# Kernel optimization log

Measured on AMD Instinct MI355X. Metric: run time of the kernel, lower is better.

Reference implementation:

```python
import jax, jax.numpy as jnp
import numpy as np

B, S, HID = 2, 2048, 2048
N_HEADS, N_KV = 16, 4
HEAD_DIM = HID // N_HEADS  # 128
N_REP = N_HEADS // N_KV
ROPE_THETA = 1000000.0


def setup_inputs() -> dict:
    key = jax.random.key(0)
    ks = jax.random.split(key, 8)
    s = 0.02
    # causal additive mask: 0 on/below diagonal, large negative above
    neg = jnp.finfo(jnp.float32).min
    causal = jnp.where(jnp.tril(jnp.ones((S, S), dtype=bool)), 0.0, neg)
    attention_mask = jnp.broadcast_to(causal[None, None], (B, 1, S, S)).astype(jnp.float32)
    return {
        "hidden_states": jax.random.normal(ks[0], (B, S, HID), jnp.float32),
        "Wq": jax.random.normal(ks[1], (HID, HID), jnp.float32) * s,
        "bq": jax.random.normal(ks[2], (HID,), jnp.float32) * s,
        "Wk": jax.random.normal(ks[3], (N_KV * HEAD_DIM, HID), jnp.float32) * s,
        "bk": jax.random.normal(ks[4], (N_KV * HEAD_DIM,), jnp.float32) * s,
        "Wv": jax.random.normal(ks[5], (N_KV * HEAD_DIM, HID), jnp.float32) * s,
        "bv": jax.random.normal(ks[6], (N_KV * HEAD_DIM,), jnp.float32) * s,
        "attention_mask": attention_mask,
        "position_ids": jnp.broadcast_to(jnp.arange(S, dtype=jnp.int64)[None], (B, S)),
    }


def _rotate_half(x):
    x1, x2 = jnp.split(x, 2, axis=-1)
    return jnp.concatenate((-x2, x1), axis=-1)


def _rope_cos_sin(position_ids, dtype):
    inv_freq = 1.0 / (ROPE_THETA ** (jnp.arange(0, HEAD_DIM, 2, dtype=jnp.float32) / HEAD_DIM))
    freqs = position_ids.astype(jnp.float32)[:, :, None] * inv_freq[None, None, :]  # [B,S,hd/2]
    emb = jnp.concatenate((freqs, freqs), axis=-1)  # [B,S,hd]
    return jnp.cos(emb).astype(dtype), jnp.sin(emb).astype(dtype)


def reference(hidden_states, Wq, bq, Wk, bk, Wv, bv, attention_mask, position_ids):
    b, s, _ = hidden_states.shape
    q = (hidden_states @ Wq.T + bq).reshape(b, s, N_HEADS, HEAD_DIM).transpose(0, 2, 1, 3)
    k = (hidden_states @ Wk.T + bk).reshape(b, s, N_KV, HEAD_DIM).transpose(0, 2, 1, 3)
    v = (hidden_states @ Wv.T + bv).reshape(b, s, N_KV, HEAD_DIM).transpose(0, 2, 1, 3)

    cos, sin = _rope_cos_sin(position_ids, hidden_states.dtype)
    cos, sin = cos[:, None], sin[:, None]  # unsqueeze head dim
    q = q * cos + _rotate_half(q) * sin
    k = k * cos + _rotate_half(k) * sin

    # GQA: repeat kv heads
    k = jnp.repeat(k, N_REP, axis=1)
    v = jnp.repeat(v, N_REP, axis=1)

    scores = jnp.einsum('bhqd,bhkd->bhqk', q, k) / jnp.sqrt(jnp.float32(HEAD_DIM)).astype(q.dtype)
    scores = scores + attention_mask
    probs = jax.nn.softmax(scores.astype(jnp.float32), axis=-1).astype(q.dtype)
    out = jnp.einsum('bhqk,bhkd->bhqd', probs, v)  # [B,H,S,hd]
    return out.transpose(0, 2, 1, 3).reshape(b, s, HID)
```

## Files before the change

### kernel.cpp

```cpp
#include <hip/hip_runtime.h>
#include <hip/hip_bf16.h>

typedef short bf16x8 __attribute__((ext_vector_type(8)));
typedef float f32x4 __attribute__((ext_vector_type(4)));
typedef unsigned int u32;
typedef unsigned short u16;

#define SLEN 2048
#define LOG2S 11

__device__ __forceinline__ u16 f2bf(float x) {
  u32 u = __builtin_bit_cast(u32, x);
  u = (u + 0x7fffu + ((u >> 16) & 1u)) >> 16;
  return (u16)u;
}

__device__ __forceinline__ u32 pkbf(float a, float b) {
  return (u32)f2bf(a) | ((u32)f2bf(b) << 16);
}

__device__ __forceinline__ void gload16(const void* g, void* l) {
  __builtin_amdgcn_global_load_lds((const __attribute__((address_space(1))) u32*)g,
                                   (__attribute__((address_space(3))) u32*)l, 16, 0, 0);
}

#define MFMA16(a, b, c) __builtin_amdgcn_mfma_f32_16x16x32_bf16((a), (b), (c), 0, 0, 0)

__global__ void k_convert4(const float* __restrict__ s0, u16* __restrict__ d0,
                           const float* __restrict__ s1, u16* __restrict__ d1,
                           const float* __restrict__ s2, u16* __restrict__ d2,
                           const float* __restrict__ s3, u16* __restrict__ d3) {
  const int n0 = 2097152, n1 = 1048576, n2 = 262144, n3 = 262144;
  const int total = n0 + n1 + n2 + n3;
  int i = blockIdx.x * blockDim.x + threadIdx.x;
  int stride = gridDim.x * blockDim.x;
  for (; i < total; i += stride) {
    const float* s; u16* d; int j = i;
    if (j < n0) { s = s0; d = d0; }
    else if ((j -= n0) < n1) { s = s1; d = d1; }
    else if ((j -= n1) < n2) { s = s2; d = d2; }
    else { j -= n2; s = s3; d = d3; }
    float4 v = reinterpret_cast<const float4*>(s)[j];
    ushort4 o;
    o.x = f2bf(v.x); o.y = f2bf(v.y); o.z = f2bf(v.z); o.w = f2bf(v.w);
    reinterpret_cast<ushort4*>(d)[j] = o;
  }
}

__global__ void k_rope_table(float* __restrict__ ctab, float* __restrict__ stab) {
  int i = blockIdx.x * blockDim.x + threadIdx.x;
  int s = i >> 6, d = i & 63;
  float invf = powf(1.0e6f, -(float)d * (1.0f / 64.0f));
  float a = (float)s * invf;
  ctab[i] = cosf(a);
  stab[i] = sinf(a);
}

__global__ __launch_bounds__(256, 2) void k_proj(
    const u16* __restrict__ Xb, const u16* __restrict__ Wqb,
    const u16* __restrict__ Wkb, const u16* __restrict__ Wvb,
    const float* __restrict__ bq, const float* __restrict__ bk, const float* __restrict__ bv,
    const float* __restrict__ ctab, const float* __restrict__ stab,
    u16* __restrict__ Qb, u16* __restrict__ Kb, u16* __restrict__ Vt) {
  __shared__ __align__(16) char smb[65536];
  const int tid = threadIdx.x;
  const int lane = tid & 63;
  const int w = tid >> 6;
  const int l15 = lane & 15, g = lane >> 4;
  const int m0 = blockIdx.x * 128;
  const int y = blockIdx.y;
  int mode, head;
  const u16* W; const float* bias;
  if (y < 16)      { mode = 0; head = y;      W = Wqb; bias = bq; }
  else if (y < 20) { mode = 1; head = y - 16; W = Wkb; bias = bk; }
  else             { mode = 2; head = y - 20; W = Wvb; bias = bv; }
  const int n0 = head * 128;

  f32x4 acc[2][8] = {};

  const char* asrc[4]; const char* bsrc[4]; int ldo[4];
  #pragma unroll
  for (int it = 0; it < 4; ++it) {
    int c = it * 256 + tid;
    int row = c >> 3;
    int inner = ((c & 7) << 4) ^ ((row & 7) << 4);
    asrc[it] = (const char*)Xb + ((size_t)(m0 + row) * 2048) * 2 + inner;
    bsrc[it] = (const char*)W  + ((size_t)(n0 + row) * 2048) * 2 + inner;
    ldo[it] = c * 16;
  }

  auto STAGE = [&](int buf, int t) {
    char* ad = smb + buf * 16384;
    char* bd = smb + 32768 + buf * 16384;
    #pragma unroll
    for (int it = 0; it < 4; ++it) gload16(asrc[it] + t * 128, ad + ldo[it]);
    #pragma unroll
    for (int it = 0; it < 4; ++it) gload16(bsrc[it] + t * 128, bd + ldo[it]);
  };

  STAGE(0, 0);
  int cur = 0;
  for (int t = 0; t < 32; ++t) {
    if (t + 1 < 32) {
      STAGE(cur ^ 1, t + 1);
      asm volatile("s_waitcnt vmcnt(8)" ::: "memory");
    } else {
      asm volatile("s_waitcnt vmcnt(0)" ::: "memory");
    }
    __builtin_amdgcn_s_barrier();
    asm volatile("" ::: "memory");
    const char* Ac = smb + cur * 16384;
    const char* Bc = smb + 32768 + cur * 16384;
    #pragma unroll
    for (int kf = 0; kf < 2; ++kf) {
      const int innerk = kf * 64 + g * 16;
      const int rowA0 = w * 32 + l15;
      const int rowA1 = rowA0 + 16;
      bf16x8 a0 = *(const bf16x8*)(Ac + rowA0 * 128 + (innerk ^ ((rowA0 & 7) << 4)));
      bf16x8 a1 = *(const bf16x8*)(Ac + rowA1 * 128 + (innerk ^ ((rowA1 & 7) << 4)));
      #pragma unroll
      for (int j = 0; j < 8; ++j) {
        const int rowB = j * 16 + l15;
        bf16x8 bb = *(const bf16x8*)(Bc + rowB * 128 + (innerk ^ ((rowB & 7) << 4)));
        acc[0][j] = MFMA16(a0, bb, acc[0][j]);
        acc[1][j] = MFMA16(a1, bb, acc[1][j]);
      }
    }
    asm volatile("" ::: "memory");
    __builtin_amdgcn_s_barrier();
    cur ^= 1;
  }

  float biasv[8];
  #pragma unroll
  for (int j = 0; j < 8; ++j) biasv[j] = bias[n0 + j * 16 + l15];

  #pragma unroll
  for (int i = 0; i < 2; ++i) {
    #pragma unroll
    for (int r = 0; r < 4; ++r) {
      const int m = m0 + w * 32 + i * 16 + g * 4 + r;
      const int b = m >> LOG2S, s = m & (SLEN - 1);
      float v[8];
      #pragma unroll
      for (int j = 0; j < 8; ++j) v[j] = acc[i][j][r] + biasv[j];
      if (mode <= 1) {
        #pragma unroll
        for (int j = 0; j < 4; ++j) {
          const int f = j * 16 + l15;
          const float cv = ctab[s * 64 + f];
          const float sv = stab[s * 64 + f];
          const float lo = v[j], hi = v[j + 4];
          v[j]     = lo * cv - hi * sv;
          v[j + 4] = hi * cv + lo * sv;
        }
      }
      if (mode == 0) {
        #pragma unroll
        for (int j = 0; j < 8; ++j) v[j] *= 0.08838834764831845f;
        u16* dst = Qb + (((size_t)(b * 16 + head) * SLEN + s) * 128);
        #pragma unroll
        for (int j = 0; j < 8; ++j) dst[j * 16 + l15] = f2bf(v[j]);
      } else if (mode == 1) {
        u16* dst = Kb + (((size_t)(b * 4 + head) * SLEN + s) * 128);
        #pragma unroll
        for (int j = 0; j < 8; ++j) dst[j * 16 + l15] = f2bf(v[j]);
      } else {
        const int sl = w * 32 + i * 16 + g * 4 + r;
        #pragma unroll
        for (int j = 0; j < 8; ++j) {
          const int d = j * 16 + l15;
          *(u16*)(smb + d * 256 + ((sl * 2) ^ ((d & 7) << 4))) = f2bf(v[j]);
        }
      }
    }
  }
  if (mode == 2) {
    __syncthreads();
    const int sbase = m0 & (SLEN - 1);
    const int bidx = m0 >> LOG2S;
    u16* Vg = Vt + ((size_t)(bidx * 4 + head) * 128) * SLEN;
    #pragma unroll
    for (int itr = 0; itr < 8; ++itr) {
      int c = itr * 256 + tid;
      int d = c >> 4, sc = c & 15;
      bf16x8 val = *(const bf16x8*)(smb + d * 256 + ((sc * 16) ^ ((d & 7) << 4)));
      *(bf16x8*)(Vg + (size_t)d * SLEN + sbase + sc * 8) = val;
    }
  }
}

__global__ __launch_bounds__(256, 3) void k_attn(
    const u16* __restrict__ Qb, const u16* __restrict__ Kb, const u16* __restrict__ Vt,
    float* __restrict__ Out) {
  __shared__ __align__(16) char smb[49152];
  const int tid = threadIdx.x, lane = tid & 63, w = tid >> 6;
  const int l15 = lane & 15, g = lane >> 4;
  const int lid = blockIdx.y * 16 + blockIdx.x;
  const int sl = lid >> 3;
  const int bh = (lid & 7) * 4 + (sl & 3);
  const int qb_t = sl >> 2;
  const int qa_t = 31 - qb_t;
  const int b = bh >> 4, h = bh & 15, kv = h >> 2;
  const u16* Qbase = Qb + ((size_t)(b * 16 + h) * SLEN) * 128;
  const char* Kg = (const char*)(Kb + ((size_t)(b * 4 + kv) * SLEN) * 128);
  const char* Vg = (const char*)(Vt + ((size_t)(b * 4 + kv) * 128) * SLEN);
  char* Pwa = smb + 32768 + w * 4096;
  char* Pwb = Pwa + 2048;

  const char* srcK[2]; const char* srcV[2]; int ldoK[2], ldoV[2];
  #pragma unroll
  for (int it = 0; it < 2; ++it) {
    int c = it * 256 + tid;
    ldoK[it] = c * 16; ldoV[it] = c * 16;
    int rk = c >> 4;
    srcK[it] = Kg + (size_t)rk * 256 + (((c & 15) << 4) ^ ((rk & 7) << 4));
    int rv = c >> 2;
    srcV[it] = Vg + (size_t)rv * (SLEN * 2) + (((c & 3) << 4) ^ (((rv >> 1) & 3) << 4));
  }

  const int qwa = qa_t * 64 + w * 16, qwb = qb_t * 64 + w * 16;
  bf16x8 qfa[4], qfb[4];
  #pragma unroll
  for (int kf = 0; kf < 4; ++kf) {
    qfa[kf] = *(const bf16x8*)(Qbase + (size_t)(qwa + l15) * 128 + kf * 32 + g * 8);
    qfb[kf] = *(const bf16x8*)(Qbase + (size_t)(qwb + l15) * 128 + kf * 32 + g * 8);
  }

  float ma = -1e30f, la = 0.f, mb = -1e30f, lb = 0.f;
  f32x4 oa[8] = {}, ob[8] = {};
  const int nt = 2 * qa_t + 2;

  auto STAGE = [&](int buf, int t) {
    char* kd = smb + buf * 8192;
    char* vd = smb + 16384 + buf * 8192;
    const size_t koK = (size_t)t * 8192;
    const size_t koV = (size_t)t * 64;
    #pragma unroll
    for (int it = 0; it < 2; ++it) gload16(srcK[it] + koK, kd + ldoK[it]);
    #pragma unroll
    for (int it = 0; it < 2; ++it) gload16(srcV[it] + koV, vd + ldoV[it]);
  };

  auto softmax = [&](f32x4* sc, float& m, float& l, f32x4* oacc, char* Pdst,
                     int k0, int qw, bool maskneed) {
    float sv[8];
    #pragma unroll
    for (int n = 0; n < 2; ++n) {
      #pragma unroll
      for (int r = 0; r < 4; ++r) {
        float x = sc[n][r];
        if (maskneed && (k0 + n * 16 + g * 4 + r > qw + l15)) x = -1e30f;
        sv[n * 4 + r] = x;
      }
    }
    float tm = fmaxf(fmaxf(fmaxf(sv[0], sv[1]), fmaxf(sv[2], sv[3])),
                     fmaxf(fmaxf(sv[4], sv[5]), fmaxf(sv[6], sv[7])));
    tm = fmaxf(tm, __shfl_xor(tm, 16));
    tm = fmaxf(tm, __shfl_xor(tm, 32));
    if (__any(tm > m + 8.0f)) {
      float mnew = fmaxf(m, tm);
      float alpha = __expf(m - mnew);
      m = mnew;
      l *= alpha;
      #pragma unroll
      for (int r = 0; r < 4; ++r) {
        float ar = __shfl(alpha, g * 4 + r);
        #pragma unroll
        for (int nf = 0; nf < 8; ++nf) oacc[nf][r] *= ar;
      }
    }
    float p[8];
    #pragma unroll
    for (int i2 = 0; i2 < 8; ++i2) p[i2] = __expf(sv[i2] - m);
    float ts = ((p[0] + p[1]) + (p[2] + p[3])) + ((p[4] + p[5]) + (p[6] + p[7]));
    ts += __shfl_xor(ts, 16);
    ts += __shfl_xor(ts, 32);
    l += ts;
    #pragma unroll
    for (int n = 0; n < 2; ++n) {
      uint2 pk;
      pk.x = pkbf(p[n * 4 + 0], p[n * 4 + 1]);
      pk.y = pkbf(p[n * 4 + 2], p[n * 4 + 3]);
      *(uint2*)(Pdst + l15 * 128 + ((n * 32 + g * 8) ^ ((l15 & 7) << 4))) = pk;
    }
  };

  STAGE(0, 0);
  int cur = 0;
  for (int t = 0; t < nt; ++t) {
    if (t + 1 < nt) {
      STAGE(cur ^ 1, t + 1);
      asm volatile("s_waitcnt vmcnt(4)" ::: "memory");
    } else {
      asm volatile("s_waitcnt vmcnt(0)" ::: "memory");
    }
    __builtin_amdgcn_s_barrier();
    asm volatile("" ::: "memory");
    const char* Kc = smb + cur * 8192;
    const char* Vc = smb + 16384 + cur * 8192;
    const int k0 = t * 32;
    const bool act_a = (k0 <= qwa + 15);
    const bool act_b = (t < 2 * qb_t + 2) && (k0 <= qwb + 15);

    if (act_a | act_b) {
      f32x4 sa[2] = {}, sb[2] = {};
      #pragma unroll
      for (int kf = 0; kf < 4; ++kf) {
        #pragma unroll
        for (int n = 0; n < 2; ++n) {
          const int row = n * 16 + l15;
          bf16x8 kb = *(const bf16x8*)(Kc + row * 256 + ((kf * 64 + g * 16) ^ ((row & 7) << 4)));
          if (act_a) sa[n] = MFMA16(kb, qfa[kf], sa[n]);
          if (act_b) sb[n] = MFMA16(kb, qfb[kf], sb[n]);
        }
      }
      if (act_a) softmax(sa, ma, la, oa, Pwa, k0, qwa, k0 + 31 > qwa);
      if (act_b) softmax(sb, mb, lb, ob, Pwb, k0, qwb, k0 + 31 > qwb);

      bf16x8 paa = {}, pab = {};
      if (act_a) paa = *(const bf16x8*)(Pwa + l15 * 128 + ((g * 16) ^ ((l15 & 7) << 4)));
      if (act_b) pab = *(const bf16x8*)(Pwb + l15 * 128 + ((g * 16) ^ ((l15 & 7) << 4)));
      #pragma unroll
      for (int nf = 0; nf < 8; ++nf) {
        const int row = nf * 16 + l15;
        bf16x8 vb = *(const bf16x8*)(Vc + row * 64 + ((g * 16) ^ (((row >> 1) & 3) << 4)));
        if (act_a) oa[nf] = MFMA16(paa, vb, oa[nf]);
        if (act_b) ob[nf] = MFMA16(pab, vb, ob[nf]);
      }
    }
    asm volatile("" ::: "memory");
    __builtin_amdgcn_s_barrier();
    cur ^= 1;
  }

  float lia = 1.0f / la, lib = 1.0f / lb;
  #pragma unroll
  for (int r = 0; r < 4; ++r) {
    float inv = __shfl(lia, g * 4 + r);
    const int q = qwa + g * 4 + r;
    float* dst = Out + ((size_t)(b * SLEN + q) * 2048) + h * 128;
    #pragma unroll
    for (int nf = 0; nf < 8; ++nf) dst[nf * 16 + l15] = oa[nf][r] * inv;
  }
  #pragma unroll
  for (int r = 0; r < 4; ++r) {
    float inv = __shfl(lib, g * 4 + r);
    const int q = qwb + g * 4 + r;
    float* dst = Out + ((size_t)(b * SLEN + q) * 2048) + h * 128;
    #pragma unroll
    for (int nf = 0; nf < 8; ++nf) dst[nf * 16 + l15] = ob[nf][r] * inv;
  }
}

extern "C" void kernel_launch(void* const* d_in, const int* in_sizes, int n_in,
                              void* d_out, int out_size, void* d_ws, size_t ws_size,
                              hipStream_t stream) {
  const float* X  = (const float*)d_in[0];
  const float* Wq = (const float*)d_in[1];
  const float* bq = (const float*)d_in[2];
  const float* Wk = (const float*)d_in[3];
  const float* bk = (const float*)d_in[4];
  const float* Wv = (const float*)d_in[5];
  const float* bv = (const float*)d_in[6];
  float* Out = (float*)d_out;
  char* ws = (char*)d_ws;
  u16* Xb    = (u16*)(ws + 0);
  u16* Wqb   = (u16*)(ws + 16777216);
  u16* Wkb   = (u16*)(ws + 25165824);
  u16* Wvb   = (u16*)(ws + 27262976);
  u16* Qb    = (u16*)(ws + 29360128);
  u16* Kb    = (u16*)(ws + 46137344);
  u16* Vt    = (u16*)(ws + 50331648);
  float* ctab = (float*)(ws + 54525952);
  float* stab = (float*)(ws + 55050240);

  hipLaunchKernelGGL(k_convert4, dim3(2048), dim3(256), 0, stream,
                     X, Xb, Wq, Wqb, Wk, Wkb, Wv, Wvb);
  hipLaunchKernelGGL(k_rope_table, dim3(512), dim3(256), 0, stream, ctab, stab);
  hipLaunchKernelGGL(k_proj, dim3(32, 24), dim3(256), 0, stream,
                     Xb, Wqb, Wkb, Wvb, bq, bk, bv, ctab, stab, Qb, Kb, Vt);
  hipLaunchKernelGGL(k_attn, dim3(16, 32), dim3(256), 0, stream, Qb, Kb, Vt, Out);
}
```

Before: 291.3 us.

## Split paired causal q-tiles into one tile per block, longest first

The attention kernel used to pair a long and a short causal query tile in each block so every block did balanced work. It now gives each block a single 64-row query tile across 1024 blocks. Blocks are ordered longest tile first, and the grid is arranged so the four query heads sharing a KV head launch next to each other for L2 reuse. The P scratch and register state are halved, so LDS drops to 36 KB and launch bounds rise to 4 blocks per CU. The cost is that each block now streams K/V without sharing it across two query tiles, which doubles K/V loads per unit of work.

```diff
diff --git a/kernel.cpp b/kernel.cpp
--- a/kernel.cpp
+++ b/kernel.cpp
@@ -190,46 +190,43 @@
   }
 }
 
-__global__ __launch_bounds__(256, 3) void k_attn(
+__global__ __launch_bounds__(256, 4) void k_attn(
     const u16* __restrict__ Qb, const u16* __restrict__ Kb, const u16* __restrict__ Vt,
     float* __restrict__ Out) {
-  __shared__ __align__(16) char smb[49152];
+  __shared__ __align__(16) char smb[36864];
   const int tid = threadIdx.x, lane = tid & 63, w = tid >> 6;
   const int l15 = lane & 15, g = lane >> 4;
-  const int lid = blockIdx.y * 16 + blockIdx.x;
-  const int sl = lid >> 3;
-  const int bh = (lid & 7) * 4 + (sl & 3);
-  const int qb_t = sl >> 2;
-  const int qa_t = 31 - qb_t;
-  const int b = bh >> 4, h = bh & 15, kv = h >> 2;
+  const int x = blockIdx.x;
+  const int y = blockIdx.y;
+  const int b = x >> 2, kv = x & 3;
+  const int hr = y & 3;
+  const int qt = 31 - (y >> 2);
+  const int h = kv * 4 + hr;
   const u16* Qbase = Qb + ((size_t)(b * 16 + h) * SLEN) * 128;
   const char* Kg = (const char*)(Kb + ((size_t)(b * 4 + kv) * SLEN) * 128);
   const char* Vg = (const char*)(Vt + ((size_t)(b * 4 + kv) * 128) * SLEN);
-  char* Pwa = smb + 32768 + w * 4096;
-  char* Pwb = Pwa + 2048;
-
-  const char* srcK[2]; const char* srcV[2]; int ldoK[2], ldoV[2];
+  char* Pw = smb + 32768 + w * 1024;
+
+  const char* srcK[2]; const char* srcV[2]; int ldo[2];
   #pragma unroll
   for (int it = 0; it < 2; ++it) {
     int c = it * 256 + tid;
-    ldoK[it] = c * 16; ldoV[it] = c * 16;
+    ldo[it] = c * 16;
     int rk = c >> 4;
     srcK[it] = Kg + (size_t)rk * 256 + (((c & 15) << 4) ^ ((rk & 7) << 4));
     int rv = c >> 2;
     srcV[it] = Vg + (size_t)rv * (SLEN * 2) + (((c & 3) << 4) ^ (((rv >> 1) & 3) << 4));
   }
 
-  const int qwa = qa_t * 64 + w * 16, qwb = qb_t * 64 + w * 16;
-  bf16x8 qfa[4], qfb[4];
-  #pragma unroll
-  for (int kf = 0; kf < 4; ++kf) {
-    qfa[kf] = *(const bf16x8*)(Qbase + (size_t)(qwa + l15) * 128 + kf * 32 + g * 8);
-    qfb[kf] = *(const bf16x8*)(Qbase + (size_t)(qwb + l15) * 128 + kf * 32 + g * 8);
-  }
-
-  float ma = -1e30f, la = 0.f, mb = -1e30f, lb = 0.f;
-  f32x4 oa[8] = {}, ob[8] = {};
-  const int nt = 2 * qa_t + 2;
+  const int qw = qt * 64 + w * 16;
+  bf16x8 qf[4];
+  #pragma unroll
+  for (int kf = 0; kf < 4; ++kf)
+    qf[kf] = *(const bf16x8*)(Qbase + (size_t)(qw + l15) * 128 + kf * 32 + g * 8);
+
+  float m = -1e30f, l = 0.f;
+  f32x4 oa[8] = {};
+  const int nt = 2 * qt + 2;
 
   auto STAGE = [&](int buf, int t) {
     char* kd = smb + buf * 8192;
@@ -237,53 +234,9 @@
     const size_t koK = (size_t)t * 8192;
     const size_t koV = (size_t)t * 64;
     #pragma unroll
-    for (int it = 0; it < 2; ++it) gload16(srcK[it] + koK, kd + ldoK[it]);
-    #pragma unroll
-    for (int it = 0; it < 2; ++it) gload16(srcV[it] + koV, vd + ldoV[it]);
-  };
-
-  auto softmax = [&](f32x4* sc, float& m, float& l, f32x4* oacc, char* Pdst,
-                     int k0, int qw, bool maskneed) {
-    float sv[8];
-    #pragma unroll
-    for (int n = 0; n < 2; ++n) {
-      #pragma unroll
-      for (int r = 0; r < 4; ++r) {
-        float x = sc[n][r];
-        if (maskneed && (k0 + n * 16 + g * 4 + r > qw + l15)) x = -1e30f;
-        sv[n * 4 + r] = x;
-      }
-    }
-    float tm = fmaxf(fmaxf(fmaxf(sv[0], sv[1]), fmaxf(sv[2], sv[3])),
-                     fmaxf(fmaxf(sv[4], sv[5]), fmaxf(sv[6], sv[7])));
-    tm = fmaxf(tm, __shfl_xor(tm, 16));
-    tm = fmaxf(tm, __shfl_xor(tm, 32));
-    if (__any(tm > m + 8.0f)) {
-      float mnew = fmaxf(m, tm);
-      float alpha = __expf(m - mnew);
-      m = mnew;
-      l *= alpha;
-      #pragma unroll
-      for (int r = 0; r < 4; ++r) {
-        float ar = __shfl(alpha, g * 4 + r);
-        #pragma unroll
-        for (int nf = 0; nf < 8; ++nf) oacc[nf][r] *= ar;
-      }
-    }
-    float p[8];
-    #pragma unroll
-    for (int i2 = 0; i2 < 8; ++i2) p[i2] = __expf(sv[i2] - m);
-    float ts = ((p[0] + p[1]) + (p[2] + p[3])) + ((p[4] + p[5]) + (p[6] + p[7]));
-    ts += __shfl_xor(ts, 16);
-    ts += __shfl_xor(ts, 32);
-    l += ts;
-    #pragma unroll
-    for (int n = 0; n < 2; ++n) {
-      uint2 pk;
-      pk.x = pkbf(p[n * 4 + 0], p[n * 4 + 1]);
-      pk.y = pkbf(p[n * 4 + 2], p[n * 4 + 3]);
-      *(uint2*)(Pdst + l15 * 128 + ((n * 32 + g * 8) ^ ((l15 & 7) << 4))) = pk;
-    }
+    for (int it = 0; it < 2; ++it) gload16(srcK[it] + koK, kd + ldo[it]);
+    #pragma unroll
+    for (int it = 0; it < 2; ++it) gload16(srcV[it] + koV, vd + ldo[it]);
   };
 
   STAGE(0, 0);
@@ -300,33 +253,65 @@
     const char* Kc = smb + cur * 8192;
     const char* Vc = smb + 16384 + cur * 8192;
     const int k0 = t * 32;
-    const bool act_a = (k0 <= qwa + 15);
-    const bool act_b = (t < 2 * qb_t + 2) && (k0 <= qwb + 15);
-
-    if (act_a | act_b) {
-      f32x4 sa[2] = {}, sb[2] = {};
+
+    if (k0 <= qw + 15) {
+      f32x4 sa[2] = {};
       #pragma unroll
       for (int kf = 0; kf < 4; ++kf) {
         #pragma unroll
         for (int n = 0; n < 2; ++n) {
           const int row = n * 16 + l15;
           bf16x8 kb = *(const bf16x8*)(Kc + row * 256 + ((kf * 64 + g * 16) ^ ((row & 7) << 4)));
-          if (act_a) sa[n] = MFMA16(kb, qfa[kf], sa[n]);
-          if (act_b) sb[n] = MFMA16(kb, qfb[kf], sb[n]);
-        }
-      }
-      if (act_a) softmax(sa, ma, la, oa, Pwa, k0, qwa, k0 + 31 > qwa);
-      if (act_b) softmax(sb, mb, lb, ob, Pwb, k0, qwb, k0 + 31 > qwb);
-
-      bf16x8 paa = {}, pab = {};
-      if (act_a) paa = *(const bf16x8*)(Pwa + l15 * 128 + ((g * 16) ^ ((l15 & 7) << 4)));
-      if (act_b) pab = *(const bf16x8*)(Pwb + l15 * 128 + ((g * 16) ^ ((l15 & 7) << 4)));
+          sa[n] = MFMA16(kb, qf[kf], sa[n]);
+        }
+      }
+      const bool maskneed = (k0 + 31 > qw);
+      float sv[8];
+      #pragma unroll
+      for (int n = 0; n < 2; ++n) {
+        #pragma unroll
+        for (int r = 0; r < 4; ++r) {
+          float xv = sa[n][r];
+          if (maskneed && (k0 + n * 16 + g * 4 + r > qw + l15)) xv = -1e30f;
+          sv[n * 4 + r] = xv;
+        }
+      }
+      float tm = fmaxf(fmaxf(fmaxf(sv[0], sv[1]), fmaxf(sv[2], sv[3])),
+                       fmaxf(fmaxf(sv[4], sv[5]), fmaxf(sv[6], sv[7])));
+      tm = fmaxf(tm, __shfl_xor(tm, 16));
+      tm = fmaxf(tm, __shfl_xor(tm, 32));
+      if (__any(tm > m + 8.0f)) {
+        float mnew = fmaxf(m, tm);
+        float alpha = __expf(m - mnew);
+        m = mnew;
+        l *= alpha;
+        #pragma unroll
+        for (int r = 0; r < 4; ++r) {
+          float ar = __shfl(alpha, g * 4 + r);
+          #pragma unroll
+          for (int nf = 0; nf < 8; ++nf) oa[nf][r] *= ar;
+        }
+      }
+      float p[8];
+      #pragma unroll
+      for (int i2 = 0; i2 < 8; ++i2) p[i2] = __expf(sv[i2] - m);
+      float ts = ((p[0] + p[1]) + (p[2] + p[3])) + ((p[4] + p[5]) + (p[6] + p[7]));
+      ts += __shfl_xor(ts, 16);
+      ts += __shfl_xor(ts, 32);
+      l += ts;
+      #pragma unroll
+      for (int n = 0; n < 2; ++n) {
+        uint2 pk;
+        pk.x = pkbf(p[n * 4 + 0], p[n * 4 + 1]);
+        pk.y = pkbf(p[n * 4 + 2], p[n * 4 + 3]);
+        *(uint2*)(Pw + l15 * 64 + ((n * 32 + g * 8) ^ ((l15 & 3) << 4))) = pk;
+      }
+      bf16x8 pa = *(const bf16x8*)(Pw + l15 * 64 + ((g * 16) ^ ((l15 & 3) << 4)));
       #pragma unroll
       for (int nf = 0; nf < 8; ++nf) {
         const int row = nf * 16 + l15;
         bf16x8 vb = *(const bf16x8*)(Vc + row * 64 + ((g * 16) ^ (((row >> 1) & 3) << 4)));
-        if (act_a) oa[nf] = MFMA16(paa, vb, oa[nf]);
-        if (act_b) ob[nf] = MFMA16(pab, vb, ob[nf]);
+        oa[nf] = MFMA16(pa, vb, oa[nf]);
       }
     }
     asm volatile("" ::: "memory");
@@ -334,22 +319,14 @@
     cur ^= 1;
   }
 
-  float lia = 1.0f / la, lib = 1.0f / lb;
+  float li = 1.0f / l;
   #pragma unroll
   for (int r = 0; r < 4; ++r) {
-    float inv = __shfl(lia, g * 4 + r);
-    const int q = qwa + g * 4 + r;
+    float inv = __shfl(li, g * 4 + r);
+    const int q = qw + g * 4 + r;
     float* dst = Out + ((size_t)(b * SLEN + q) * 2048) + h * 128;
     #pragma unroll
     for (int nf = 0; nf < 8; ++nf) dst[nf * 16 + l15] = oa[nf][r] * inv;
-  }
-  #pragma unroll
-  for (int r = 0; r < 4; ++r) {
-    float inv = __shfl(lib, g * 4 + r);
-    const int q = qwb + g * 4 + r;
-    float* dst = Out + ((size_t)(b * SLEN + q) * 2048) + h * 128;
-    #pragma unroll
-    for (int nf = 0; nf < 8; ++nf) dst[nf * 16 + l15] = ob[nf][r] * inv;
   }
 }
 
@@ -380,5 +357,5 @@
   hipLaunchKernelGGL(k_rope_table, dim3(512), dim3(256), 0, stream, ctab, stab);
   hipLaunchKernelGGL(k_proj, dim3(32, 24), dim3(256), 0, stream,
                      Xb, Wqb, Wkb, Wvb, bq, bk, bv, ctab, stab, Qb, Kb, Vt);
-  hipLaunchKernelGGL(k_attn, dim3(16, 32), dim3(256), 0, stream, Qb, Kb, Vt, Out);
-}
+  hipLaunchKernelGGL(k_attn, dim3(8, 128), dim3(256), 0, stream, Qb, Kb, Vt, Out);
+}
```

Measured after the change: 265.6 us. -8.8%, faster.
